# Kernel tuning notes

Hardware: AMD Instinct MI355X
Metric: run time of the kernel (lower is better)

The kernel has to match this reference:

```python
import jax, jax.numpy as jnp
import numpy as np
import math

N_EMBD = 1024
N_HEAD = 16
HEAD_DIM = N_EMBD // N_HEAD
# Faithful to source: scores = QK^T / scale, where scale = 1/sqrt(head_dim)
# => scores = QK^T * sqrt(head_dim)
INV_SCALE = math.sqrt(HEAD_DIM)


def setup_inputs() -> dict:
    key = jax.random.key(0)
    ks = jax.random.split(key, 9)
    B, S = 4, 2048
    x = jax.random.normal(ks[0], (B, S, N_EMBD), dtype=jnp.float32)
    init = 1.0 / math.sqrt(N_EMBD)
    def lin(kw, kb):
        W = jax.random.uniform(kw, (N_EMBD, N_EMBD), jnp.float32, -init, init)
        b = jax.random.uniform(kb, (N_EMBD,), jnp.float32, -init, init)
        return W, b
    Wq, bq = lin(ks[1], ks[2])
    Wk, bk = lin(ks[3], ks[4])
    Wv, bv = lin(ks[5], ks[6])
    Wo, bo = lin(ks[7], ks[8])
    return {"x": x, "Wq": Wq, "bq": bq, "Wk": Wk, "bk": bk,
            "Wv": Wv, "bv": bv, "Wo": Wo, "bo": bo}


def reference(x, Wq, bq, Wk, bk, Wv, bv, Wo, bo):
    B, S, _ = x.shape
    # projections (torch Linear: y = x @ W^T + b; here weights stored [in,out])
    q = (x @ Wq + bq).reshape(B, S, N_HEAD, HEAD_DIM)
    k = (x @ Wk + bk).reshape(B, S, N_HEAD, HEAD_DIM)
    v = (x @ Wv + bv).reshape(B, S, N_HEAD, HEAD_DIM)
    # scores: [B, H, S, S]; note unusual scaling (divide by 1/sqrt(d))
    scores = jnp.einsum('bqhd,bkhd->bhqk', q, k) * INV_SCALE
    attn = jax.nn.softmax(scores, axis=-1)
    # dropout in eval mode -> identity
    out = jnp.einsum('bhqk,bkhd->bqhd', attn, v).reshape(B, S, N_EMBD)
    return out @ Wo + bo
```

## Files before the change

kernel.cpp:

```cpp
#include <hip/hip_runtime.h>
#include <hip/hip_bf16.h>

#define DEVI static __device__ __forceinline__

typedef __attribute__((ext_vector_type(8))) _Float16 f16x8;
typedef __attribute__((ext_vector_type(2))) __fp16 fp16v2;
typedef __attribute__((ext_vector_type(4))) float f32x4;
typedef __attribute__((ext_vector_type(16))) float f32x16;
typedef __attribute__((ext_vector_type(8))) unsigned short u16x8;
typedef __attribute__((ext_vector_type(4))) unsigned int u32x4;
typedef __attribute__((ext_vector_type(2))) unsigned int u32x2;
typedef unsigned short u16;

constexpr int NE = 1024;
constexpr int NH = 16;
constexpr int HD = 64;
constexpr int SB = 4;
constexpr int SS = 2048;
constexpr int MR = SB * SS;

DEVI u16 f2h(float f) {
  union { _Float16 h; u16 u; } x;
  x.h = (_Float16)f;
  return x.u;
}

DEVI unsigned pk2(float lo, float hi) {
  union { fp16v2 h2; unsigned u; } cv;
  cv.h2 = __builtin_amdgcn_cvt_pkrtz(lo, hi);
  return cv.u;
}

DEVI void gload_lds16(const void* g, void* l) {
  __builtin_amdgcn_global_load_lds(
      (const __attribute__((address_space(1))) unsigned int*)g,
      (__attribute__((address_space(3))) unsigned int*)l, 16, 0, 0);
}

__global__ void k_cvt_x(const float* __restrict__ x, u16* __restrict__ xb) {
  size_t i = (size_t)blockIdx.x * 256 + threadIdx.x;
  const f32x4* s4 = (const f32x4*)x;
  f32x4 a = s4[2 * i], c = s4[2 * i + 1];
  u16x8 o;
  o[0] = f2h(a[0]); o[1] = f2h(a[1]); o[2] = f2h(a[2]); o[3] = f2h(a[3]);
  o[4] = f2h(c[0]); o[5] = f2h(c[1]); o[6] = f2h(c[2]); o[7] = f2h(c[3]);
  ((u16x8*)xb)[i] = o;
}

__global__ void k_wt(const float* __restrict__ W0, const float* __restrict__ W1,
                     const float* __restrict__ W2, const float* __restrict__ W3,
                     u16* __restrict__ WT) {
  __shared__ float tile[64][65];
  const float* W = (blockIdx.z == 0) ? W0 : (blockIdx.z == 1) ? W1 : (blockIdx.z == 2) ? W2 : W3;
  u16* T = WT + (size_t)blockIdx.z * NE * NE;
  int tid = threadIdx.x, c = tid & 63, rr = tid >> 6;
  int ti = blockIdx.y * 64, tj = blockIdx.x * 64;
#pragma unroll
  for (int p = 0; p < 16; p++) {
    int r = p * 4 + rr;
    tile[r][c] = W[(size_t)(ti + r) * NE + tj + c];
  }
  __syncthreads();
#pragma unroll
  for (int p = 0; p < 16; p++) {
    int r = p * 4 + rr;
    T[(size_t)(tj + r) * NE + ti + c] = f2h(tile[c][r]);
  }
}

template <int MODE>
__global__ __launch_bounds__(256) void k_gemm(const u16* __restrict__ A,
                                              const u16* __restrict__ BT,
                                              const float* __restrict__ bias,
                                              void* __restrict__ outp) {
  __shared__ __align__(16) u16 lA[128 * 64];
  __shared__ __align__(16) u16 lB[128 * 64];
  const int tid = threadIdx.x;
  const int wave = tid >> 6, lane = tid & 63;
  const int wr = wave >> 1, wc = wave & 1;
  const int fr = lane & 15, fg = lane >> 4;
  const int srow = lane >> 3;
  const int scol = ((lane & 7) ^ srow) * 8;
  const int mb = blockIdx.x, nb = blockIdx.y;
  f32x4 acc[4][4] = {};
  for (int kt = 0; kt < NE / 64; ++kt) {
#pragma unroll
    for (int p = 0; p < 4; p++) {
      int rb = wave * 32 + p * 8;
      gload_lds16(A + (size_t)(mb * 128 + rb + srow) * NE + kt * 64 + scol, lA + rb * 64);
      gload_lds16(BT + (size_t)(nb * 128 + rb + srow) * NE + kt * 64 + scol, lB + rb * 64);
    }
    __syncthreads();
#pragma unroll
    for (int kd = 0; kd < 2; ++kd) {
      f16x8 af[4], bg[4];
#pragma unroll
      for (int mi = 0; mi < 4; mi++) {
        int row = wr * 64 + mi * 16 + fr;
        af[mi] = *(const f16x8*)((const char*)lA + row * 128 + ((kd * 64 + fg * 16) ^ ((row & 7) << 4)));
      }
#pragma unroll
      for (int nj = 0; nj < 4; nj++) {
        int row = wc * 64 + nj * 16 + fr;
        bg[nj] = *(const f16x8*)((const char*)lB + row * 128 + ((kd * 64 + fg * 16) ^ ((row & 7) << 4)));
      }
#pragma unroll
      for (int mi = 0; mi < 4; mi++)
#pragma unroll
        for (int nj = 0; nj < 4; nj++)
          acc[mi][nj] = __builtin_amdgcn_mfma_f32_16x16x32_f16(af[mi], bg[nj], acc[mi][nj], 0, 0, 0);
    }
    __syncthreads();
  }
  float bv[4];
#pragma unroll
  for (int nj = 0; nj < 4; nj++) bv[nj] = bias[nb * 128 + wc * 64 + nj * 16 + fr];
#pragma unroll
  for (int mi = 0; mi < 4; mi++)
#pragma unroll
    for (int nj = 0; nj < 4; nj++)
#pragma unroll
      for (int r = 0; r < 4; r++) {
        int row = mb * 128 + wr * 64 + mi * 16 + fg * 4 + r;
        int col = nb * 128 + wc * 64 + nj * 16 + fr;
        float v = acc[mi][nj][r] + bv[nj];
        if constexpr (MODE == 2) {
          ((float*)outp)[(size_t)row * NE + col] = v;
        } else if constexpr (MODE == 0) {
          ((u16*)outp)[(size_t)row * NE + col] = f2h(v);
        } else {
          int b = row >> 11, s = row & (SS - 1);
          int h = col >> 6, d = col & 63;
          ((u16*)outp)[(((size_t)(b * NH + h) * HD + d) << 11) | (size_t)s] = f2h(v);
        }
      }
}

__global__ __launch_bounds__(256) void k_attn(const u16* __restrict__ Q, const u16* __restrict__ K,
                                              const u16* __restrict__ VT, u16* __restrict__ AO) {
  __shared__ __align__(16) u16 smem[4 * 4096];
  const int tid = threadIdx.x, wave = tid >> 6, lane = tid & 63;
  const int q32 = lane & 31, hh = lane >> 5;
  const int srow = lane >> 3;
  const int scol = ((lane & 7) ^ srow) * 8;
  const int qb = blockIdx.x * 128, h = blockIdx.y, b = blockIdx.z;
  const u16* Kg = K + (size_t)(b * SS) * NE + h * HD;
  const u16* Vg = VT + (size_t)(b * NH + h) * HD * SS;
  const u16* Qp = Q + (size_t)(b * SS + qb + wave * 32 + q32) * NE + h * HD;
  f16x8 qf[4];
#pragma unroll
  for (int m = 0; m < 4; m++) qf[m] = *(const f16x8*)(Qp + m * 16 + hh * 8);
  f32x16 oacc[2] = {};
  float m_s = -1e30f, l_s = 0.f;
  const float SC = 8.0f * 1.44269504088896340736f;

  auto STAGE = [&](int kt2, int bufi) {
    u16* lk = smem + bufi * 4096;
    u16* lv = smem + 8192 + bufi * 4096;
#pragma unroll
    for (int p = 0; p < 2; p++) {
      int rb = wave * 16 + p * 8;
      gload_lds16(Kg + (size_t)(kt2 * 64 + rb + srow) * NE + scol, lk + rb * 64);
      gload_lds16(Vg + (size_t)(rb + srow) * SS + kt2 * 64 + scol, lv + rb * 64);
    }
  };

  STAGE(0, 0);
  for (int kt = 0; kt < SS / 64; ++kt) {
    const int cur = kt & 1;
    __syncthreads();
    if (kt + 1 < SS / 64) STAGE(kt + 1, cur ^ 1);
    const u16* lk = smem + cur * 4096;
    const u16* lv = smem + 8192 + cur * 4096;
    f32x16 sacc[2];
#pragma unroll
    for (int kt32 = 0; kt32 < 2; kt32++) {
      f32x16 z = {};
      int row = kt32 * 32 + q32;
      __builtin_amdgcn_s_setprio(1);
#pragma unroll
      for (int m = 0; m < 4; m++) {
        f16x8 kf = *(const f16x8*)((const char*)lk + row * 128 + ((m * 32 + hh * 16) ^ ((row & 7) << 4)));
        z = __builtin_amdgcn_mfma_f32_32x32x16_f16(kf, qf[m], z, 0, 0, 0);
      }
      __builtin_amdgcn_s_setprio(0);
      sacc[kt32] = z;
    }
    float a[16];
#pragma unroll
    for (int r = 0; r < 16; r++) a[r] = fmaxf(sacc[0][r], sacc[1][r]);
#pragma unroll
    for (int s = 8; s > 0; s >>= 1)
#pragma unroll
      for (int r = 0; r < s; r++) a[r] = fmaxf(a[r], a[r + s]);
    float mx = a[0] * SC;
    mx = fmaxf(mx, __shfl_xor(mx, 32));
    float mo = m_s, mu = mo;
    if (!__all(mx <= mo + 8.f)) {
      float nm = fmaxf(mo, mx);
      float fs = __builtin_amdgcn_exp2f(mo - nm);
      m_s = nm; mu = nm; l_s *= fs;
#pragma unroll
      for (int d2 = 0; d2 < 2; d2++)
#pragma unroll
        for (int r = 0; r < 16; r++) oacc[d2][r] *= fs;
    }
    float p[2][16];
#pragma unroll
    for (int kt32 = 0; kt32 < 2; kt32++)
#pragma unroll
      for (int r = 0; r < 16; r++)
        p[kt32][r] = __builtin_amdgcn_exp2f(sacc[kt32][r] * SC - mu);
    float t[16];
#pragma unroll
    for (int r = 0; r < 16; r++) t[r] = p[0][r] + p[1][r];
#pragma unroll
    for (int s = 8; s > 0; s >>= 1)
#pragma unroll
      for (int r = 0; r < s; r++) t[r] += t[r + s];
    float rs = t[0];
    rs += __shfl_xor(rs, 32);
    l_s += rs;
    unsigned W[2][4][2];
#pragma unroll
    for (int kt32 = 0; kt32 < 2; kt32++)
#pragma unroll
      for (int aa = 0; aa < 4; aa++)
#pragma unroll
        for (int b2 = 0; b2 < 2; b2++)
          W[kt32][aa][b2] = pk2(p[kt32][4 * aa + 2 * b2], p[kt32][4 * aa + 2 * b2 + 1]);
    unsigned bw[4][4];
#pragma unroll
    for (int kt32 = 0; kt32 < 2; kt32++)
#pragma unroll
      for (int tau = 0; tau < 2; tau++)
#pragma unroll
        for (int b2 = 0; b2 < 2; b2++) {
          u32x2 r2 = __builtin_amdgcn_permlane32_swap(W[kt32][2 * tau][b2], W[kt32][2 * tau + 1][b2],
                                                      false, false);
          int tt = kt32 * 2 + tau;
          bw[tt][b2]     = r2[0];
          bw[tt][b2 + 2] = r2[1];
        }
    f16x8 pf[4];
#pragma unroll
    for (int tt = 0; tt < 4; tt++) {
      union { unsigned w[4]; f16x8 v; } u;
#pragma unroll
      for (int w = 0; w < 4; w++) u.w[w] = bw[tt][w];
      pf[tt] = u.v;
    }
#pragma unroll
    for (int d2 = 0; d2 < 2; d2++) {
      int row = d2 * 32 + q32;
      __builtin_amdgcn_s_setprio(1);
#pragma unroll
      for (int tt = 0; tt < 4; tt++) {
        f16x8 vf = *(const f16x8*)((const char*)lv + row * 128 + ((tt * 32 + hh * 16) ^ ((row & 7) << 4)));
        oacc[d2] = __builtin_amdgcn_mfma_f32_32x32x16_f16(vf, pf[tt], oacc[d2], 0, 0, 0);
      }
      __builtin_amdgcn_s_setprio(0);
    }
  }
  __syncthreads();
  unsigned* epi = (unsigned*)smem + wave * (32 * 36);
  float inv = 1.0f / l_s;
#pragma unroll
  for (int d2 = 0; d2 < 2; d2++)
#pragma unroll
    for (int aa = 0; aa < 4; aa++)
#pragma unroll
      for (int b2 = 0; b2 < 2; b2++) {
        int r0 = 4 * aa + 2 * b2;
        epi[q32 * 36 + d2 * 16 + 4 * aa + 2 * hh + b2] =
            pk2(oacc[d2][r0] * inv, oacc[d2][r0 + 1] * inv);
      }
  __syncthreads();
  {
    int q2 = lane >> 1, part = lane & 1;
    const unsigned* src = (const unsigned*)smem + wave * (32 * 36) + q2 * 36 + part * 16;
    u16* dst = AO + (size_t)(b * SS + qb + wave * 32 + q2) * NE + h * HD + part * 32;
#pragma unroll
    for (int u = 0; u < 4; u++)
      *(u32x4*)(dst + u * 8) = *(const u32x4*)(src + u * 4);
  }
}

extern "C" void kernel_launch(void* const* d_in, const int* in_sizes, int n_in,
                              void* d_out, int out_size, void* d_ws, size_t ws_size,
                              hipStream_t stream) {
  const float* x  = (const float*)d_in[0];
  const float* Wq = (const float*)d_in[1]; const float* bq = (const float*)d_in[2];
  const float* Wk = (const float*)d_in[3]; const float* bk = (const float*)d_in[4];
  const float* Wv = (const float*)d_in[5]; const float* bv = (const float*)d_in[6];
  const float* Wo = (const float*)d_in[7]; const float* bo = (const float*)d_in[8];

  u16* xb  = (u16*)d_ws;
  u16* WT  = xb  + (size_t)MR * NE;
  u16* Qb  = WT  + (size_t)4 * NE * NE;
  u16* Kb  = Qb  + (size_t)MR * NE;
  u16* VTb = Kb  + (size_t)MR * NE;
  u16* AOb = xb;

  k_cvt_x<<<dim3(MR * NE / (256 * 8)), 256, 0, stream>>>(x, xb);
  k_wt<<<dim3(16, 16, 4), 256, 0, stream>>>(Wq, Wk, Wv, Wo, WT);

  dim3 gg(MR / 128, NE / 128);
  k_gemm<0><<<gg, 256, 0, stream>>>(xb, WT + 0 * (size_t)NE * NE, bq, Qb);
  k_gemm<0><<<gg, 256, 0, stream>>>(xb, WT + 1 * (size_t)NE * NE, bk, Kb);
  k_gemm<1><<<gg, 256, 0, stream>>>(xb, WT + 2 * (size_t)NE * NE, bv, VTb);

  k_attn<<<dim3(SS / 128, NH, SB), 256, 0, stream>>>(Qb, Kb, VTb, AOb);

  k_gemm<2><<<gg, 256, 0, stream>>>(AOb, WT + 3 * (size_t)NE * NE, bo, (float*)d_out);
}
```

Baseline: 224.1 us.

## Triple-buffer attention K/V and overlap next QK with softmax, add XCD-aware block mapping

Restructures the attention main loop into a software pipeline with three LDS buffers. The QK^T MFMA for the next tile is issued before the softmax and PV of the previous tile, so matrix work overlaps the exp/reduction work. The grid is also flattened and remapped so blocks of the same batch/head land on the same XCD, to improve L2 reuse of K/V. LDS use grows to 48KB per block and register pressure rises from holding two score tiles, which may lower occupancy.

```diff
diff --git a/kernel.cpp b/kernel.cpp
--- a/kernel.cpp
+++ b/kernel.cpp
@@ -138,12 +138,16 @@
 
 __global__ __launch_bounds__(256) void k_attn(const u16* __restrict__ Q, const u16* __restrict__ K,
                                               const u16* __restrict__ VT, u16* __restrict__ AO) {
-  __shared__ __align__(16) u16 smem[4 * 4096];
+  __shared__ __align__(16) u16 smem[6 * 4096];
   const int tid = threadIdx.x, wave = tid >> 6, lane = tid & 63;
   const int q32 = lane & 31, hh = lane >> 5;
   const int srow = lane >> 3;
   const int scol = ((lane & 7) ^ srow) * 8;
-  const int qb = blockIdx.x * 128, h = blockIdx.y, b = blockIdx.z;
+  const int bid = blockIdx.x;
+  const int xcd = bid & 7, idx = bid >> 3;
+  const int g = xcd * 8 + (idx >> 4);
+  const int qb = (idx & 15) * 128;
+  const int b = g >> 4, h = g & 15;
   const u16* Kg = K + (size_t)(b * SS) * NE + h * HD;
   const u16* Vg = VT + (size_t)(b * NH + h) * HD * SS;
   const u16* Qp = Q + (size_t)(b * SS + qb + wave * 32 + q32) * NE + h * HD;
@@ -156,7 +160,7 @@
 
   auto STAGE = [&](int kt2, int bufi) {
     u16* lk = smem + bufi * 4096;
-    u16* lv = smem + 8192 + bufi * 4096;
+    u16* lv = smem + 12288 + bufi * 4096;
 #pragma unroll
     for (int p = 0; p < 2; p++) {
       int rb = wave * 16 + p * 8;
@@ -165,14 +169,8 @@
     }
   };
 
-  STAGE(0, 0);
-  for (int kt = 0; kt < SS / 64; ++kt) {
-    const int cur = kt & 1;
-    __syncthreads();
-    if (kt + 1 < SS / 64) STAGE(kt + 1, cur ^ 1);
-    const u16* lk = smem + cur * 4096;
-    const u16* lv = smem + 8192 + cur * 4096;
-    f32x16 sacc[2];
+  auto QK = [&](int bufi, f32x16* s) {
+    const u16* lk = smem + bufi * 4096;
 #pragma unroll
     for (int kt32 = 0; kt32 < 2; kt32++) {
       f32x16 z = {};
@@ -184,15 +182,19 @@
         z = __builtin_amdgcn_mfma_f32_32x32x16_f16(kf, qf[m], z, 0, 0, 0);
       }
       __builtin_amdgcn_s_setprio(0);
-      sacc[kt32] = z;
-    }
+      s[kt32] = z;
+    }
+  };
+
+  auto SMPV = [&](int bufiV, f32x16* s) {
+    const u16* lv = smem + 12288 + bufiV * 4096;
     float a[16];
 #pragma unroll
-    for (int r = 0; r < 16; r++) a[r] = fmaxf(sacc[0][r], sacc[1][r]);
-#pragma unroll
-    for (int s = 8; s > 0; s >>= 1)
-#pragma unroll
-      for (int r = 0; r < s; r++) a[r] = fmaxf(a[r], a[r + s]);
+    for (int r = 0; r < 16; r++) a[r] = fmaxf(s[0][r], s[1][r]);
+#pragma unroll
+    for (int st = 8; st > 0; st >>= 1)
+#pragma unroll
+      for (int r = 0; r < st; r++) a[r] = fmaxf(a[r], a[r + st]);
     float mx = a[0] * SC;
     mx = fmaxf(mx, __shfl_xor(mx, 32));
     float mo = m_s, mu = mo;
@@ -210,34 +212,27 @@
     for (int kt32 = 0; kt32 < 2; kt32++)
 #pragma unroll
       for (int r = 0; r < 16; r++)
-        p[kt32][r] = __builtin_amdgcn_exp2f(sacc[kt32][r] * SC - mu);
+        p[kt32][r] = __builtin_amdgcn_exp2f(s[kt32][r] * SC - mu);
     float t[16];
 #pragma unroll
     for (int r = 0; r < 16; r++) t[r] = p[0][r] + p[1][r];
 #pragma unroll
-    for (int s = 8; s > 0; s >>= 1)
-#pragma unroll
-      for (int r = 0; r < s; r++) t[r] += t[r + s];
+    for (int st = 8; st > 0; st >>= 1)
+#pragma unroll
+      for (int r = 0; r < st; r++) t[r] += t[r + st];
     float rs = t[0];
     rs += __shfl_xor(rs, 32);
     l_s += rs;
-    unsigned W[2][4][2];
+    unsigned bw[4][4];
 #pragma unroll
     for (int kt32 = 0; kt32 < 2; kt32++)
 #pragma unroll
-      for (int aa = 0; aa < 4; aa++)
-#pragma unroll
-        for (int b2 = 0; b2 < 2; b2++)
-          W[kt32][aa][b2] = pk2(p[kt32][4 * aa + 2 * b2], p[kt32][4 * aa + 2 * b2 + 1]);
-    unsigned bw[4][4];
-#pragma unroll
-    for (int kt32 = 0; kt32 < 2; kt32++)
-#pragma unroll
       for (int tau = 0; tau < 2; tau++)
 #pragma unroll
         for (int b2 = 0; b2 < 2; b2++) {
-          u32x2 r2 = __builtin_amdgcn_permlane32_swap(W[kt32][2 * tau][b2], W[kt32][2 * tau + 1][b2],
-                                                      false, false);
+          unsigned Y = pk2(p[kt32][4 * (2 * tau) + 2 * b2],     p[kt32][4 * (2 * tau) + 2 * b2 + 1]);
+          unsigned X = pk2(p[kt32][4 * (2 * tau + 1) + 2 * b2], p[kt32][4 * (2 * tau + 1) + 2 * b2 + 1]);
+          u32x2 r2 = __builtin_amdgcn_permlane32_swap(Y, X, false, false);
           int tt = kt32 * 2 + tau;
           bw[tt][b2]     = r2[0];
           bw[tt][b2 + 2] = r2[1];
@@ -261,7 +256,28 @@
       }
       __builtin_amdgcn_s_setprio(0);
     }
-  }
+  };
+
+  f32x16 sA[2], sB[2];
+  STAGE(0, 0);
+  STAGE(1, 1);
+  __syncthreads();
+  QK(0, sA);
+  for (int t = 1; t < 31; t += 2) {
+    __syncthreads();
+    STAGE(t + 1, (t + 1) % 3);
+    QK(t % 3, sB);
+    SMPV((t - 1) % 3, sA);
+    __syncthreads();
+    STAGE(t + 2, (t + 2) % 3);
+    QK((t + 1) % 3, sA);
+    SMPV(t % 3, sB);
+  }
+  __syncthreads();
+  QK(31 % 3, sB);
+  SMPV(30 % 3, sA);
+  SMPV(31 % 3, sB);
+
   __syncthreads();
   unsigned* epi = (unsigned*)smem + wave * (32 * 36);
   float inv = 1.0f / l_s;
@@ -310,7 +326,7 @@
   k_gemm<0><<<gg, 256, 0, stream>>>(xb, WT + 1 * (size_t)NE * NE, bk, Kb);
   k_gemm<1><<<gg, 256, 0, stream>>>(xb, WT + 2 * (size_t)NE * NE, bv, VTb);
 
-  k_attn<<<dim3(SS / 128, NH, SB), 256, 0, stream>>>(Qb, Kb, VTb, AOb);
+  k_attn<<<dim3(1024), 256, 0, stream>>>(Qb, Kb, VTb, AOb);
 
   k_gemm<2><<<gg, 256, 0, stream>>>(AOb, WT + 3 * (size_t)NE * NE, bo, (float*)d_out);
 }
```

Result: no change. 222.1 us (-0.9%).
